# Optimization experiments

Measured on AMD Instinct MI355X. Metric: run time of the kernel, lower is better.

The kernel has to match this reference:

```python
import jax, jax.numpy as jnp
import numpy as np

B, T, IN, OUT = 4, 8192, 512, 512
DIM, G, V, D = 32, 8, 8, 64  # quantizer dim, groups, num_vars, var_dim (vq_dim//groups)
TAU = 2.0  # initial gumbel temperature temp[0]
EPS = 1e-10


def setup_inputs() -> dict:
    key = jax.random.key(0)
    ks = jax.random.split(key, 8)
    s = lambda k, sh, f: (jax.random.normal(k, sh, jnp.float32) * f)
    return {
        "x": s(ks[0], (B, T, IN), 1.0),
        "W_pre": s(ks[1], (IN, DIM), IN ** -0.5),
        "b_pre": jnp.zeros((DIM,), jnp.float32),
        "W_proj": s(ks[2], (DIM, G * V), DIM ** -0.5),
        "b_proj": jnp.zeros((G * V,), jnp.float32),
        "codebook": s(ks[3], (G, V, D), 1.0),
        "W_post": s(ks[4], (G * D, OUT), (G * D) ** -0.5),
        "b_post": jnp.zeros((OUT,), jnp.float32),
        "u": jax.random.uniform(ks[5], (B, T, G, V), jnp.float32),
    }


def reference(x, W_pre, b_pre, W_proj, b_proj, codebook, W_post, b_post, u):
    b, t, _ = x.shape
    g, v, d = codebook.shape
    # pre-projection to quantizer dim, then logits over groups x num_vars
    h = x @ W_pre + b_pre                                # (B,T,32)
    logits = (h @ W_proj + b_proj).reshape(b, t, g, v)   # (B,T,G,V)
    # gumbel-softmax (hard, straight-through) as in F.gumbel_softmax
    gum = -jnp.log(-jnp.log(u + EPS) + EPS)
    y_soft = jax.nn.softmax((logits + gum) / TAU, axis=-1)
    hard = jax.nn.one_hot(jnp.argmax(y_soft, axis=-1), v, dtype=y_soft.dtype)
    w = hard + y_soft - jax.lax.stop_gradient(y_soft)    # (B,T,G,V)
    # codebook lookup: weighted sum over num_vars per group, concat groups
    q = jnp.einsum("btgv,gvd->btgd", w, codebook).reshape(b, t, g * d)
    return q @ W_post + b_post                           # (B,T,OUT)
```

## Files before the change

kernel.cpp:

```cpp
#include <hip/hip_runtime.h>
#include <hip/hip_bf16.h>
#include <stdint.h>
#include <stddef.h>

#define BT_TOK   32768
#define IN_DIM   512
#define OUT_DIM  512
#define QDIM     32
#define NG       8
#define NV       8
#define VD       64
#define EPS_G    1e-10f

#define MT       64
#define NW       8

__global__ __launch_bounds__(256) void build_p2(
    const float* __restrict__ codebook,
    const float* __restrict__ W_post,
    __hip_bfloat16* __restrict__ P2)
{
    const int b  = blockIdx.x;
    const int p  = b >> 6;
    const int ij = b & 63;
    const int i  = ij >> 3, j = ij & 7;
    const int t  = threadIdx.x;

    const float* ca  = codebook + ((size_t)(2 * p) * NV + i) * VD;
    const float* cbp = codebook + ((size_t)(2 * p + 1) * NV + j) * VD;
    const float* wa  = W_post + (size_t)(2 * p) * VD * OUT_DIM;
    const float* wb  = W_post + (size_t)(2 * p + 1) * VD * OUT_DIM;

    float a0 = 0.f, a1 = 0.f;
#pragma unroll 8
    for (int d = 0; d < VD; ++d) {
        const float sa = ca[d];
        const float sb = cbp[d];
        a0 += sa * wa[(size_t)d * OUT_DIM + t]       + sb * wb[(size_t)d * OUT_DIM + t];
        a1 += sa * wa[(size_t)d * OUT_DIM + t + 256] + sb * wb[(size_t)d * OUT_DIM + t + 256];
    }
    __hip_bfloat16* dst = P2 + ((size_t)(p * 64 + ij)) * OUT_DIM;
    dst[t]       = __float2bfloat16(a0);
    dst[t + 256] = __float2bfloat16(a1);
}

__global__ __launch_bounds__(512, 4) void fused_main(
    const float* __restrict__ x,
    const float* __restrict__ W_pre,
    const float* __restrict__ b_pre,
    const float* __restrict__ W_proj,
    const float* __restrict__ b_proj,
    const float* __restrict__ u,
    const float* __restrict__ b_post,
    const __hip_bfloat16* __restrict__ P2,
    float* __restrict__ out)
{
    __shared__ float Hs4[NW][MT][36];
    __shared__ int   idxs_s[NG][MT];
    __shared__ int   pidx_s[4][MT];

    const int t    = threadIdx.x;
    const int lane = t & 63;
    const int w    = __builtin_amdgcn_readfirstlane(t >> 6);
    const int tokbase = blockIdx.x * MT;
    const int gtok    = tokbase + lane;

    float acc[QDIM];
#pragma unroll
    for (int j = 0; j < QDIM; ++j) acc[j] = 0.f;

    const float* xrow = x + (size_t)gtok * IN_DIM + w * 64;

#pragma unroll
    for (int c = 0; c < 2; ++c) {
        float4 xr[8];
#pragma unroll
        for (int f = 0; f < 8; ++f)
            xr[f] = ((const float4*)xrow)[c * 8 + f];

        const float* wbase = W_pre + (size_t)(w * 64 + c * 32) * QDIM;
#pragma unroll
        for (int kk = 0; kk < 32; ++kk) {
            const float xv = ((const float*)xr)[kk];
            const float4* wr = (const float4*)(wbase + (size_t)kk * QDIM);
            const float4 w0 = wr[0], w1 = wr[1], w2 = wr[2], w3 = wr[3];
            const float4 w4 = wr[4], w5 = wr[5], w6 = wr[6], w7 = wr[7];
            acc[0]  += xv * w0.x; acc[1]  += xv * w0.y; acc[2]  += xv * w0.z; acc[3]  += xv * w0.w;
            acc[4]  += xv * w1.x; acc[5]  += xv * w1.y; acc[6]  += xv * w1.z; acc[7]  += xv * w1.w;
            acc[8]  += xv * w2.x; acc[9]  += xv * w2.y; acc[10] += xv * w2.z; acc[11] += xv * w2.w;
            acc[12] += xv * w3.x; acc[13] += xv * w3.y; acc[14] += xv * w3.z; acc[15] += xv * w3.w;
            acc[16] += xv * w4.x; acc[17] += xv * w4.y; acc[18] += xv * w4.z; acc[19] += xv * w4.w;
            acc[20] += xv * w5.x; acc[21] += xv * w5.y; acc[22] += xv * w5.z; acc[23] += xv * w5.w;
            acc[24] += xv * w6.x; acc[25] += xv * w6.y; acc[26] += xv * w6.z; acc[27] += xv * w6.w;
            acc[28] += xv * w7.x; acc[29] += xv * w7.y; acc[30] += xv * w7.z; acc[31] += xv * w7.w;
        }
    }

#pragma unroll
    for (int j4 = 0; j4 < 8; ++j4)
        *(float4*)&Hs4[w][lane][j4 * 4] =
            make_float4(acc[j4 * 4], acc[j4 * 4 + 1], acc[j4 * 4 + 2], acc[j4 * 4 + 3]);
    __syncthreads();

#pragma unroll
    for (int r = 0; r < 4; ++r) {
        const int id  = t + 512 * r;
        const int tok = id >> 5;
        const int j   = id & 31;
        float h = b_pre[j];
#pragma unroll
        for (int q = 0; q < NW; ++q) h += Hs4[q][tok][j];
        Hs4[0][tok][j] = h;
    }
    __syncthreads();

    float h[QDIM];
#pragma unroll
    for (int j4 = 0; j4 < 8; ++j4) {
        const float4 v = *(const float4*)&Hs4[0][lane][j4 * 4];
        h[j4 * 4] = v.x; h[j4 * 4 + 1] = v.y; h[j4 * 4 + 2] = v.z; h[j4 * 4 + 3] = v.w;
    }

    {
        const int g = w;
        const float4 b0 = *(const float4*)&b_proj[g * 8];
        const float4 b1 = *(const float4*)&b_proj[g * 8 + 4];
        float lg[8] = {b0.x, b0.y, b0.z, b0.w, b1.x, b1.y, b1.z, b1.w};

#pragma unroll
        for (int j = 0; j < QDIM; ++j) {
            const float hv = h[j];
            const float4 a0 = *(const float4*)&W_proj[(size_t)j * 64 + g * 8];
            const float4 a1 = *(const float4*)&W_proj[(size_t)j * 64 + g * 8 + 4];
            lg[0] += hv * a0.x; lg[1] += hv * a0.y; lg[2] += hv * a0.z; lg[3] += hv * a0.w;
            lg[4] += hv * a1.x; lg[5] += hv * a1.y; lg[6] += hv * a1.z; lg[7] += hv * a1.w;
        }

        const float4 u0 = *(const float4*)&u[(size_t)gtok * 64 + g * 8];
        const float4 u1 = *(const float4*)&u[(size_t)gtok * 64 + g * 8 + 4];
        float y[8];
        y[0] = lg[0] - logf(-logf(u0.x + EPS_G) + EPS_G);
        y[1] = lg[1] - logf(-logf(u0.y + EPS_G) + EPS_G);
        y[2] = lg[2] - logf(-logf(u0.z + EPS_G) + EPS_G);
        y[3] = lg[3] - logf(-logf(u0.w + EPS_G) + EPS_G);
        y[4] = lg[4] - logf(-logf(u1.x + EPS_G) + EPS_G);
        y[5] = lg[5] - logf(-logf(u1.y + EPS_G) + EPS_G);
        y[6] = lg[6] - logf(-logf(u1.z + EPS_G) + EPS_G);
        y[7] = lg[7] - logf(-logf(u1.w + EPS_G) + EPS_G);

        float best = y[0];
        int bi = 0;
#pragma unroll
        for (int v = 1; v < 8; ++v)
            if (y[v] > best) { best = y[v]; bi = v; }
        idxs_s[g][lane] = bi;
    }
    __syncthreads();

    if (t < 256) {
        const int p = t >> 6, tok = t & 63;
        pidx_s[p][tok] = idxs_s[2 * p][tok] * 8 + idxs_s[2 * p + 1][tok];
    }
    __syncthreads();

    const int tokhalf = t >> 8;
    const int tt = t & 255;
    const int o2 = tt * 2;
    const float bp0 = b_post[o2];
    const float bp1 = b_post[o2 + 1];
    float* orow = out + (size_t)(tokbase + tokhalf * 32) * OUT_DIM;
    const uint32_t* p2u = (const uint32_t*)P2;

#pragma unroll 4
    for (int tok0 = 0; tok0 < 32; ++tok0) {
        const int tok = tokhalf * 32 + tok0;
        const int p0 = pidx_s[0][tok];
        const int p1 = pidx_s[1][tok];
        const int p2i = pidx_s[2][tok];
        const int p3 = pidx_s[3][tok];
        const uint32_t r0 = p2u[(size_t)(0 * 64 + p0) * 256 + tt];
        const uint32_t r1 = p2u[(size_t)(1 * 64 + p1) * 256 + tt];
        const uint32_t r2 = p2u[(size_t)(2 * 64 + p2i) * 256 + tt];
        const uint32_t r3 = p2u[(size_t)(3 * 64 + p3) * 256 + tt];
        float s0 = bp0, s1 = bp1;
        s0 += __uint_as_float(r0 << 16); s1 += __uint_as_float(r0 & 0xffff0000u);
        s0 += __uint_as_float(r1 << 16); s1 += __uint_as_float(r1 & 0xffff0000u);
        s0 += __uint_as_float(r2 << 16); s1 += __uint_as_float(r2 & 0xffff0000u);
        s0 += __uint_as_float(r3 << 16); s1 += __uint_as_float(r3 & 0xffff0000u);
        *(float2*)&orow[(size_t)tok0 * OUT_DIM + o2] = make_float2(s0, s1);
    }
}

extern "C" void kernel_launch(void* const* d_in, const int* in_sizes, int n_in,
                              void* d_out, int out_size, void* d_ws, size_t ws_size,
                              hipStream_t stream) {
    const float* x        = (const float*)d_in[0];
    const float* W_pre    = (const float*)d_in[1];
    const float* b_pre    = (const float*)d_in[2];
    const float* W_proj   = (const float*)d_in[3];
    const float* b_proj   = (const float*)d_in[4];
    const float* codebook = (const float*)d_in[5];
    const float* W_post   = (const float*)d_in[6];
    const float* b_post   = (const float*)d_in[7];
    const float* u        = (const float*)d_in[8];
    float* out = (float*)d_out;

    __hip_bfloat16* P2 = (__hip_bfloat16*)d_ws;

    build_p2<<<256, 256, 0, stream>>>(codebook, W_post, P2);
    fused_main<<<BT_TOK / MT, 512, 0, stream>>>(x, W_pre, b_pre, W_proj, b_proj,
                                                u, b_post, P2, out);
}
```

Baseline: 160.2 us.

## Split fused kernel into logits and gather kernels, coalesce x loads via LDS

Splits the fused kernel in two. The first kernel computes the pre-projection, logits and gumbel argmax, and writes one packed 32-bit index word per token to the workspace. The second kernel gathers the precomputed bf16 codebook-projection rows and writes the output with nontemporal stores. The x loads are restructured so each wave reads contiguous row segments and transposes them through shared memory, replacing the per-lane strided row reads. This costs an extra kernel launch and a small round trip through global memory in exchange for coalesced reads and smaller, higher-occupancy blocks for the output stage.

```diff
diff --git a/kernel.cpp b/kernel.cpp
--- a/kernel.cpp
+++ b/kernel.cpp
@@ -14,6 +14,8 @@
 
 #define MT       64
 #define NW       8
+
+typedef float f32x2 __attribute__((ext_vector_type(2)));
 
 __global__ __launch_bounds__(256) void build_p2(
     const float* __restrict__ codebook,
@@ -44,20 +46,17 @@
     dst[t + 256] = __float2bfloat16(a1);
 }
 
-__global__ __launch_bounds__(512, 4) void fused_main(
+__global__ __launch_bounds__(512, 4) void fused_logits(
     const float* __restrict__ x,
     const float* __restrict__ W_pre,
     const float* __restrict__ b_pre,
     const float* __restrict__ W_proj,
     const float* __restrict__ b_proj,
     const float* __restrict__ u,
-    const float* __restrict__ b_post,
-    const __hip_bfloat16* __restrict__ P2,
-    float* __restrict__ out)
+    uint32_t* __restrict__ pidx_pack)
 {
     __shared__ float Hs4[NW][MT][36];
     __shared__ int   idxs_s[NG][MT];
-    __shared__ int   pidx_s[4][MT];
 
     const int t    = threadIdx.x;
     const int lane = t & 63;
@@ -69,30 +68,40 @@
 #pragma unroll
     for (int j = 0; j < QDIM; ++j) acc[j] = 0.f;
 
-    const float* xrow = x + (size_t)gtok * IN_DIM + w * 64;
-
-#pragma unroll
-    for (int c = 0; c < 2; ++c) {
-        float4 xr[8];
-#pragma unroll
-        for (int f = 0; f < 8; ++f)
-            xr[f] = ((const float4*)xrow)[c * 8 + f];
-
-        const float* wbase = W_pre + (size_t)(w * 64 + c * 32) * QDIM;
-#pragma unroll
-        for (int kk = 0; kk < 32; ++kk) {
-            const float xv = ((const float*)xr)[kk];
-            const float4* wr = (const float4*)(wbase + (size_t)kk * QDIM);
-            const float4 w0 = wr[0], w1 = wr[1], w2 = wr[2], w3 = wr[3];
-            const float4 w4 = wr[4], w5 = wr[5], w6 = wr[6], w7 = wr[7];
-            acc[0]  += xv * w0.x; acc[1]  += xv * w0.y; acc[2]  += xv * w0.z; acc[3]  += xv * w0.w;
-            acc[4]  += xv * w1.x; acc[5]  += xv * w1.y; acc[6]  += xv * w1.z; acc[7]  += xv * w1.w;
-            acc[8]  += xv * w2.x; acc[9]  += xv * w2.y; acc[10] += xv * w2.z; acc[11] += xv * w2.w;
-            acc[12] += xv * w3.x; acc[13] += xv * w3.y; acc[14] += xv * w3.z; acc[15] += xv * w3.w;
-            acc[16] += xv * w4.x; acc[17] += xv * w4.y; acc[18] += xv * w4.z; acc[19] += xv * w4.w;
-            acc[20] += xv * w5.x; acc[21] += xv * w5.y; acc[22] += xv * w5.z; acc[23] += xv * w5.w;
-            acc[24] += xv * w6.x; acc[25] += xv * w6.y; acc[26] += xv * w6.z; acc[27] += xv * w6.w;
-            acc[28] += xv * w7.x; acc[29] += xv * w7.y; acc[30] += xv * w7.z; acc[31] += xv * w7.w;
+    const int tsub = lane >> 3;
+    const int c4   = lane & 7;
+    const float* xws = x + (size_t)tokbase * IN_DIM + w * 64;
+
+#pragma unroll
+    for (int s = 0; s < 2; ++s) {
+        float4 xv[8];
+#pragma unroll
+        for (int i = 0; i < 8; ++i)
+            xv[i] = *(const float4*)(xws + (size_t)(i * 8 + tsub) * IN_DIM + s * 32 + c4 * 4);
+#pragma unroll
+        for (int i = 0; i < 8; ++i)
+            *(float4*)&Hs4[w][i * 8 + tsub][c4 * 4] = xv[i];
+
+        const float* wbase = W_pre + (size_t)(w * 64 + s * 32) * QDIM;
+#pragma unroll
+        for (int k4 = 0; k4 < 8; ++k4) {
+            const float4 xr = *(const float4*)&Hs4[w][lane][k4 * 4];
+            const float xk4[4] = {xr.x, xr.y, xr.z, xr.w};
+#pragma unroll
+            for (int e = 0; e < 4; ++e) {
+                const float xvv = xk4[e];
+                const float4* wr = (const float4*)(wbase + (size_t)(k4 * 4 + e) * QDIM);
+                const float4 w0 = wr[0], w1 = wr[1], w2 = wr[2], w3 = wr[3];
+                const float4 w4 = wr[4], w5 = wr[5], w6 = wr[6], w7 = wr[7];
+                acc[0]  += xvv * w0.x; acc[1]  += xvv * w0.y; acc[2]  += xvv * w0.z; acc[3]  += xvv * w0.w;
+                acc[4]  += xvv * w1.x; acc[5]  += xvv * w1.y; acc[6]  += xvv * w1.z; acc[7]  += xvv * w1.w;
+                acc[8]  += xvv * w2.x; acc[9]  += xvv * w2.y; acc[10] += xvv * w2.z; acc[11] += xvv * w2.w;
+                acc[12] += xvv * w3.x; acc[13] += xvv * w3.y; acc[14] += xvv * w3.z; acc[15] += xvv * w3.w;
+                acc[16] += xvv * w4.x; acc[17] += xvv * w4.y; acc[18] += xvv * w4.z; acc[19] += xvv * w4.w;
+                acc[20] += xvv * w5.x; acc[21] += xvv * w5.y; acc[22] += xvv * w5.z; acc[23] += xvv * w5.w;
+                acc[24] += xvv * w6.x; acc[25] += xvv * w6.y; acc[26] += xvv * w6.z; acc[27] += xvv * w6.w;
+                acc[28] += xvv * w7.x; acc[29] += xvv * w7.y; acc[30] += xvv * w7.z; acc[31] += xvv * w7.w;
+            }
         }
     }
 
@@ -157,37 +166,49 @@
     }
     __syncthreads();
 
-    if (t < 256) {
-        const int p = t >> 6, tok = t & 63;
-        pidx_s[p][tok] = idxs_s[2 * p][tok] * 8 + idxs_s[2 * p + 1][tok];
-    }
-    __syncthreads();
-
-    const int tokhalf = t >> 8;
-    const int tt = t & 255;
-    const int o2 = tt * 2;
+    if (t < MT) {
+        const int tok = t;
+        const uint32_t pk =
+              (uint32_t)(idxs_s[0][tok] * 8 + idxs_s[1][tok])
+            | ((uint32_t)(idxs_s[2][tok] * 8 + idxs_s[3][tok]) << 8)
+            | ((uint32_t)(idxs_s[4][tok] * 8 + idxs_s[5][tok]) << 16)
+            | ((uint32_t)(idxs_s[6][tok] * 8 + idxs_s[7][tok]) << 24);
+        pidx_pack[tokbase + tok] = pk;
+    }
+}
+
+__global__ __launch_bounds__(256) void gather_out(
+    const uint32_t* __restrict__ pidx_pack,
+    const float* __restrict__ b_post,
+    const __hip_bfloat16* __restrict__ P2,
+    float* __restrict__ out)
+{
+    __shared__ uint32_t pp[32];
+    const int t = threadIdx.x;
+    const int tokbase = blockIdx.x * 32;
+    if (t < 32) pp[t] = pidx_pack[tokbase + t];
+    __syncthreads();
+
+    const int o2 = t * 2;
     const float bp0 = b_post[o2];
     const float bp1 = b_post[o2 + 1];
-    float* orow = out + (size_t)(tokbase + tokhalf * 32) * OUT_DIM;
     const uint32_t* p2u = (const uint32_t*)P2;
+    float* obase = out + (size_t)tokbase * OUT_DIM + o2;
 
 #pragma unroll 4
-    for (int tok0 = 0; tok0 < 32; ++tok0) {
-        const int tok = tokhalf * 32 + tok0;
-        const int p0 = pidx_s[0][tok];
-        const int p1 = pidx_s[1][tok];
-        const int p2i = pidx_s[2][tok];
-        const int p3 = pidx_s[3][tok];
-        const uint32_t r0 = p2u[(size_t)(0 * 64 + p0) * 256 + tt];
-        const uint32_t r1 = p2u[(size_t)(1 * 64 + p1) * 256 + tt];
-        const uint32_t r2 = p2u[(size_t)(2 * 64 + p2i) * 256 + tt];
-        const uint32_t r3 = p2u[(size_t)(3 * 64 + p3) * 256 + tt];
+    for (int tok = 0; tok < 32; ++tok) {
+        const uint32_t pk = pp[tok];
+        const uint32_t r0 = p2u[(size_t)((pk      ) & 63) * 256 + t];
+        const uint32_t r1 = p2u[(size_t)(64  + ((pk >> 8 ) & 63)) * 256 + t];
+        const uint32_t r2 = p2u[(size_t)(128 + ((pk >> 16) & 63)) * 256 + t];
+        const uint32_t r3 = p2u[(size_t)(192 + ((pk >> 24) & 63)) * 256 + t];
         float s0 = bp0, s1 = bp1;
         s0 += __uint_as_float(r0 << 16); s1 += __uint_as_float(r0 & 0xffff0000u);
         s0 += __uint_as_float(r1 << 16); s1 += __uint_as_float(r1 & 0xffff0000u);
         s0 += __uint_as_float(r2 << 16); s1 += __uint_as_float(r2 & 0xffff0000u);
         s0 += __uint_as_float(r3 << 16); s1 += __uint_as_float(r3 & 0xffff0000u);
-        *(float2*)&orow[(size_t)tok0 * OUT_DIM + o2] = make_float2(s0, s1);
+        f32x2 sv; sv.x = s0; sv.y = s1;
+        __builtin_nontemporal_store(sv, (f32x2*)(obase + (size_t)tok * OUT_DIM));
     }
 }
 
@@ -206,8 +227,10 @@
     float* out = (float*)d_out;
 
     __hip_bfloat16* P2 = (__hip_bfloat16*)d_ws;
+    uint32_t* pidx     = (uint32_t*)((char*)d_ws + 256 * 1024);
 
     build_p2<<<256, 256, 0, stream>>>(codebook, W_post, P2);
-    fused_main<<<BT_TOK / MT, 512, 0, stream>>>(x, W_pre, b_pre, W_proj, b_proj,
-                                                u, b_post, P2, out);
-}
+    fused_logits<<<BT_TOK / MT, 512, 0, stream>>>(x, W_pre, b_pre, W_proj, b_proj,
+                                                  u, pidx);
+    gather_out<<<BT_TOK / 32, 256, 0, stream>>>(pidx, b_post, P2, out);
+}
```

After: 156.5 us. -2.3%, faster.
